# Performance work log

Measured on AMD Instinct MI355X. Metric: run time of the kernel, lower is better.

The kernel has to match this reference:

```python
import jax, jax.numpy as jnp
import numpy as np

NC = 3
NA = 3
NO2D = NC + 5
BIN = 2
NO3D = BIN * 3 + 3
STRIDES = (8.0, 16.0, 32.0)
ANCHORS = np.array([[10, 13, 16, 30, 33, 23],
                    [30, 61, 62, 45, 59, 119],
                    [116, 90, 156, 198, 373, 326]], np.float32).reshape(3, NA, 2)
IN_CHES = (256, 512, 1024)
SIZES = ((80, 80), (40, 40), (20, 20))
BS = 8


def _conv(x, w, b, pad):
    y = jax.lax.conv_general_dilated(x, w, (1, 1), ((pad, pad), (pad, pad)),
                                     dimension_numbers=('NCHW', 'OIHW', 'NCHW'))
    return y + b[None, :, None, None]


def setup_inputs() -> dict:
    key = jax.random.key(0)
    d = {}
    k = [0]
    def nk():
        k[0] += 1
        return jax.random.fold_in(key, k[0])
    for i, (c, (ny, nx)) in enumerate(zip(IN_CHES, SIZES)):
        d[f"f{i}"] = jax.random.normal(nk(), (BS, c, ny, nx), jnp.float32)
        d[f"w2a{i}"] = jax.random.normal(nk(), (c, c, 3, 3), jnp.float32) * 0.01
        d[f"b2a{i}"] = jnp.zeros((c,), jnp.float32)
        d[f"w2b{i}"] = jax.random.normal(nk(), (NA * NO2D, c, 1, 1), jnp.float32) * 0.01
        d[f"b2b{i}"] = jnp.zeros((NA * NO2D,), jnp.float32)
        d[f"w3a{i}"] = jax.random.normal(nk(), (c, c, 3, 3), jnp.float32) * 0.01
        d[f"b3a{i}"] = jnp.zeros((c,), jnp.float32)
        d[f"w3b{i}"] = jax.random.normal(nk(), (NA * NO3D, c, 1, 1), jnp.float32) * 0.01
        d[f"b3b{i}"] = jnp.zeros((NA * NO3D,), jnp.float32)
    return d


def _decode(feats, params):
    anchors = jnp.asarray(ANCHORS)  # [L, NA, 2]
    preds = []
    for i in range(3):
        x = feats[i]
        w2a, b2a, w2b, b2b, w3a, b3a, w3b, b3b = params[i]
        # detection heads: 3x3 conv -> 1x1 conv
        h2 = _conv(_conv(x, w2a, b2a, 1), w2b, b2b, 0)  # [bs, na*NO2D, ny, nx]
        h3 = _conv(_conv(x, w3a, b3a, 1), w3b, b3b, 0)  # [bs, na*NO3D, ny, nx]
        bs, _, ny, nx = h2.shape
        h2 = h2.reshape(bs, NA, NO2D, ny, nx).transpose(0, 1, 3, 4, 2)  # [bs,na,ny,nx,NO2D]
        h3 = h3.reshape(bs, NA, NO3D, ny, nx).transpose(0, 1, 3, 4, 2).reshape(bs, -1, NO3D)
        # 2d decode
        p2 = jax.nn.sigmoid(h2)
        yv, xv = jnp.meshgrid(jnp.arange(ny, dtype=jnp.float32),
                              jnp.arange(nx, dtype=jnp.float32), indexing='ij')
        grid = jnp.stack((xv, yv), -1)[None, None]  # [1,1,ny,nx,2]
        xy = (p2[..., 0:2] * 2.0 - 0.5 + grid) * STRIDES[i]
        wh = (p2[..., 2:4] * 2.0) ** 2 * anchors[i][None, :, None, None, :]
        p2 = jnp.concatenate([xy, wh, p2[..., 4:]], -1).reshape(bs, -1, NO2D)
        # 3d decode: bin confidences raw, bin orients L2-normalized, dims sigmoid*2-1
        bins = h3[..., :BIN]
        orient = h3[..., BIN:3 * BIN].reshape(bs, -1, BIN, 2)
        norm = jnp.maximum(jnp.linalg.norm(orient, axis=-1, keepdims=True), 1e-12)
        orient = (orient / norm).reshape(bs, -1, BIN * 2)
        dims = jax.nn.sigmoid(h3[..., -3:]) * 2.0 - 1.0
        p3 = jnp.concatenate([bins, orient, dims], -1)
        preds.append(jnp.concatenate([p2, p3], -1))
    return jnp.concatenate(preds, 1)  # [bs, 25200, NO2D+NO3D]


def reference(f0, f1, f2,
              w2a0, b2a0, w2b0, b2b0, w3a0, b3a0, w3b0, b3b0,
              w2a1, b2a1, w2b1, b2b1, w3a1, b3a1, w3b1, b3b1,
              w2a2, b2a2, w2b2, b2b2, w3a2, b3a2, w3b2, b3b2):
    feats = (f0, f1, f2)
    params = ((w2a0, b2a0, w2b0, b2b0, w3a0, b3a0, w3b0, b3b0),
              (w2a1, b2a1, w2b1, b2b1, w3a1, b3a1, w3b1, b3b1),
              (w2a2, b2a2, w2b2, b2b2, w3a2, b3a2, w3b2, b3b2))
    return _decode(feats, params)
```

## Files before the change

### kernel.cpp

```cpp
#include <hip/hip_runtime.h>
#include <hip/hip_bf16.h>
#include <cstddef>
#include <cstdint>
#include <climits>

#define TOT_ANCH 25200

typedef __bf16 bf16x8 __attribute__((ext_vector_type(8)));
typedef float f32x4 __attribute__((ext_vector_type(4)));

__device__ __forceinline__ float sig_(float x) { return 1.0f / (1.0f + __expf(-x)); }

__device__ __forceinline__ short f2bf(float v) {
  return (short)__builtin_bit_cast(unsigned short, __float2bfloat16(v));
}
__device__ __forceinline__ float bf2f(short v) {
  unsigned int u = ((unsigned int)(unsigned short)v) << 16;
  return __builtin_bit_cast(float, u);
}
__device__ __forceinline__ bf16x8 as_bf16x8(int4 v) { return __builtin_bit_cast(bf16x8, v); }

__device__ __forceinline__ void gload_lds16(const void* g, void* l) {
  __builtin_amdgcn_global_load_lds((const __attribute__((address_space(1))) void*)g,
                                   (__attribute__((address_space(3))) void*)l, 16, 0, 0);
}

__device__ const float d_anch[3][3][2] = {
    {{10.f, 13.f}, {16.f, 30.f}, {33.f, 23.f}},
    {{30.f, 61.f}, {62.f, 45.f}, {59.f, 119.f}},
    {{116.f, 90.f}, {156.f, 198.f}, {373.f, 326.f}}};

struct TrP {
  const float* f; short* fb; int C, HW, ptiles, c32, blk0;
};
struct WtP {
  const float* w; short* dst; long CC, MC, off0; int blk0;
};
struct WcP {
  const float* w2b; const float* w3b; short* wc; int csh2, blk0;
};
struct ConvP {
  const short* fb; const short* wt; const float* bA; const float* bB; short* h;
  int C, H, W, HW, nb_m, nwg, mfast, blk0;
};
struct DeP {
  const short* h; const short* wc; const float* bb2; const float* bb3;
  int C2, H, W, b0, loff, ptiles, lvl, blk0; float stride;
};

__global__ __launch_bounds__(256) void aux_mega(TrP T0, TrP T1, TrP T2,
                                                WtP J0, WtP J1, WtP J2,
                                                WtP J3, WtP J4, WtP J5, int wt_blk0) {
  __shared__ short tile[32][33];
  int bid = blockIdx.x;
  if (bid >= wt_blk0) {
    WtP J = bid >= J5.blk0 ? J5 : bid >= J4.blk0 ? J4 : bid >= J3.blk0 ? J3 :
            bid >= J2.blk0 ? J2 : bid >= J1.blk0 ? J1 : J0;
    long oi = (long)(bid - J.blk0) * 256 + threadIdx.x;
    if (oi >= J.CC) return;
#pragma unroll
    for (int t = 0; t < 9; ++t) J.dst[t * J.MC + J.off0 + oi] = f2bf(J.w[oi * 9 + t]);
    return;
  }
  TrP T = bid >= T2.blk0 ? T2 : (bid >= T1.blk0 ? T1 : T0);
  int l = bid - T.blk0;
  const int pt = l % T.ptiles; l /= T.ptiles;
  const int cg = l % T.c32;
  const int b = l / T.c32;
  const int p0 = pt * 32, c0 = cg * 32, HW = T.HW, C = T.C;
  const int t = threadIdx.x;
  {
    int cl = t >> 3, pl = (t & 7) * 4;
    int pr = p0 + pl;
    if (pr > HW - 4) pr = HW - 4;
    const float4 v = *(const float4*)(T.f + ((long)b * C + c0 + cl) * HW + pr);
    tile[cl][pl + 0] = f2bf(v.x);
    tile[cl][pl + 1] = f2bf(v.y);
    tile[cl][pl + 2] = f2bf(v.z);
    tile[cl][pl + 3] = f2bf(v.w);
  }
  __syncthreads();
  {
    int pl = t >> 3, cl = (t & 7) * 4;
    int pp = p0 + pl;
    if (pp < HW) {
      int k = pl >> 2;
      int start = p0 + 4 * k;
      if (start > HW - 4) start = HW - 4;
      int col = (start - p0) + (pp - start);
      short4 o;
      o.x = tile[cl + 0][col];
      o.y = tile[cl + 1][col];
      o.z = tile[cl + 2][col];
      o.w = tile[cl + 3][col];
      *(short4*)(T.fb + ((long)b * HW + pp) * C + c0 + cl) = o;
    }
  }
}

__global__ __launch_bounds__(256) void wc_prep(WcP K0, WcP K1, WcP K2) {
  int bid = blockIdx.x;
  WcP K = bid >= K2.blk0 ? K2 : (bid >= K1.blk0 ? K1 : K0);
  int idx = (bid - K.blk0) * 256 + threadIdx.x;
  const int C2 = 1 << K.csh2;
  if (idx >= 64 * C2) return;
  const int row = idx >> K.csh2;
  const int c = idx & (C2 - 1);
  const int C = C2 >> 1;
  float v = 0.f;
  if (row < 24) {
    if (c < C) v = K.w2b[row * C + c];
  } else if (row < 51) {
    if (c >= C) v = K.w3b[(row - 24) * C + (c - C)];
  }
  K.wc[idx] = f2bf(v);
}

__global__ __launch_bounds__(256, 3) void conv3x3_mega(ConvP P0, ConvP P1, ConvP P2,
                                                       const short* zbuf) {
  __shared__ __align__(16) short As[128 * 64];
  __shared__ __align__(16) short Xs[128 * 64];

  int bid = blockIdx.x;
  ConvP P = bid >= P2.blk0 ? P2 : (bid >= P1.blk0 ? P1 : P0);
  const int C = P.C, H = P.H, W = P.W, HW = P.HW, nb_m = P.nb_m, nwg = P.nwg;

  const int orig = bid - P.blk0;
  const int q = nwg >> 3, rr = nwg & 7;
  const int xcd = orig & 7;
  const int wg = (xcd < rr ? xcd * (q + 1) : rr * (q + 1) + (xcd - rr) * q) + (orig >> 3);
  int m, n;
  if (P.mfast) { m = wg % nb_m; n = wg / nb_m; }
  else         { const int nb_n = nwg / nb_m; n = wg % nb_n; m = wg / nb_n; }
  const int mt0 = m * 128;
  const int nt0 = n * 128;
  const int M2 = nb_m * 128;

  const int tid = threadIdx.x;
  const int lane = tid & 63;
  const int wave = tid >> 6;
  const int wm = (wave >> 1) * 64;
  const int wn = (wave & 1) * 64;
  const int s = tid & 7;

  int xs_x[4], xs_y[4];
  int xs_base[4];
  int as_base[4];
#pragma unroll
  for (int r = 0; r < 4; ++r) {
    int cl = r * 32 + (tid >> 3);
    int nn = nt0 + cl;
    int b = nn / HW; int p = nn - b * HW;
    int y = p / W;  int x = p - y * W;
    xs_x[r] = x; xs_y[r] = y;
    int swz = (s ^ (cl & 7)) * 8;
    xs_base[r] = ((b * H + y) * W + x) * C + swz;
    as_base[r] = (mt0 + cl) * C + swz;
  }

  f32x4 acc[4][4];
#pragma unroll
  for (int a_ = 0; a_ < 4; ++a_)
#pragma unroll
    for (int b_ = 0; b_ < 4; ++b_) acc[a_][b_] = (f32x4){0.f, 0.f, 0.f, 0.f};

  const int nkb = C >> 6;
  const long MC = (long)M2 * C;
  const short* gzb = zbuf + s * 8;

  for (int kb = 0; kb < nkb; ++kb) {
    const int kb64 = kb << 6;
    for (int t = 0; t < 9; ++t) {
      const int dy = t / 3 - 1, dx = t - (t / 3) * 3 - 1;
      const int doff = (dy * W + dx) * C + kb64;
      const short* gap = P.wt + (long)t * MC + kb64;
#pragma unroll
      for (int r = 0; r < 4; ++r) {
        gload_lds16(gap + as_base[r], (char*)As + r * 4096 + tid * 16);
        bool ok = ((unsigned)(xs_y[r] + dy) < (unsigned)H) &
                  ((unsigned)(xs_x[r] + dx) < (unsigned)W);
        const short* gx = ok ? P.fb + xs_base[r] + doff : gzb;
        gload_lds16(gx, (char*)Xs + r * 4096 + tid * 16);
      }
      __syncthreads();

#pragma unroll
      for (int ks = 0; ks < 2; ++ks) {
        bf16x8 af[4], xf[4];
#pragma unroll
        for (int mf = 0; mf < 4; ++mf) {
          int row = wm + mf * 16 + (lane & 15);
          int c = (ks * 4 + (lane >> 4)) ^ (row & 7);
          af[mf] = as_bf16x8(*(const int4*)((const char*)As + row * 128 + c * 16));
        }
#pragma unroll
        for (int nf = 0; nf < 4; ++nf) {
          int col = wn + nf * 16 + (lane & 15);
          int c = (ks * 4 + (lane >> 4)) ^ (col & 7);
          xf[nf] = as_bf16x8(*(const int4*)((const char*)Xs + col * 128 + c * 16));
        }
        __builtin_amdgcn_s_setprio(1);
#pragma unroll
        for (int mf = 0; mf < 4; ++mf)
#pragma unroll
          for (int nf = 0; nf < 4; ++nf)
            acc[mf][nf] = __builtin_amdgcn_mfma_f32_16x16x32_bf16(af[mf], xf[nf],
                                                                  acc[mf][nf], 0, 0, 0);
        __builtin_amdgcn_s_setprio(0);
      }
      __syncthreads();
    }
  }

  long nbase[4];
#pragma unroll
  for (int nf = 0; nf < 4; ++nf) {
    int nn = nt0 + wn + nf * 16 + (lane & 15);
    int nb = nn / HW;
    int np = nn - nb * HW;
    nbase[nf] = ((long)nb * HW + np) * M2;
  }
#pragma unroll
  for (int mf = 0; mf < 4; ++mf) {
    int co0 = mt0 + wm + mf * 16 + (lane >> 4) * 4;
    float bv[4];
#pragma unroll
    for (int rg = 0; rg < 4; ++rg) {
      int co = co0 + rg;
      bv[rg] = co < C ? P.bA[co] : P.bB[co - C];
    }
#pragma unroll
    for (int nf = 0; nf < 4; ++nf) {
      short4 o;
      o.x = f2bf(acc[mf][nf][0] + bv[0]);
      o.y = f2bf(acc[mf][nf][1] + bv[1]);
      o.z = f2bf(acc[mf][nf][2] + bv[2]);
      o.w = f2bf(acc[mf][nf][3] + bv[3]);
      *(short4*)(P.h + nbase[nf] + co0) = o;
    }
  }
}

__global__ __launch_bounds__(256) void decode_v3(DeP D0, DeP D1, DeP D2,
                                                 float* __restrict__ out) {
  __shared__ __align__(16) short htileT[32][136];
  __shared__ __align__(16) short Wtile[64][136];
  __shared__ float otile[32][52];
  int bid = blockIdx.x;
  DeP D = bid >= D2.blk0 ? D2 : (bid >= D1.blk0 ? D1 : D0);
  int l = bid - D.blk0;
  const int pt = l % D.ptiles;
  const int bl = l / D.ptiles;
  const int C2 = D.C2, H = D.H, W = D.W, HW = H * W;
  const int t = threadIdx.x;
  const int lane = t & 63;
  const int wv = t >> 6;
  const int p0 = pt * 32;

  const short* hB = D.h + (long)bl * HW * C2;

  f32x4 acc[2];
  acc[0] = (f32x4){0.f, 0.f, 0.f, 0.f};
  acc[1] = (f32x4){0.f, 0.f, 0.f, 0.f};

  const int rounds = C2 >> 7;
  for (int rd = 0; rd < rounds; ++rd) {
    const int c0 = rd << 7;
#pragma unroll
    for (int r = 0; r < 2; ++r) {
      int idx = r * 256 + t;
      int px = idx >> 4, kc = idx & 15;
      int p = p0 + px;
      int pc = p < HW ? p : HW - 1;
      int4 v = *(const int4*)(hB + (long)pc * C2 + c0 + kc * 8);
      *(int4*)&htileT[px][kc * 8] = v;
    }
#pragma unroll
    for (int r = 0; r < 4; ++r) {
      int idx = r * 256 + t;
      int row = idx >> 4, kc = idx & 15;
      int4 v = *(const int4*)(D.wc + (long)row * C2 + c0 + kc * 8);
      *(int4*)&Wtile[row][kc * 8] = v;
    }
    __syncthreads();
#pragma unroll
    for (int st = 0; st < 4; ++st) {
      const int k0 = st * 32 + (lane >> 4) * 8;
      bf16x8 af = as_bf16x8(*(const int4*)&Wtile[wv * 16 + (lane & 15)][k0]);
#pragma unroll
      for (int nf = 0; nf < 2; ++nf) {
        bf16x8 xf = as_bf16x8(*(const int4*)&htileT[nf * 16 + (lane & 15)][k0]);
        acc[nf] = __builtin_amdgcn_mfma_f32_16x16x32_bf16(af, xf, acc[nf], 0, 0, 0);
      }
    }
    __syncthreads();
  }

#pragma unroll
  for (int nf = 0; nf < 2; ++nf) {
    int px = nf * 16 + (lane & 15);
#pragma unroll
    for (int rg = 0; rg < 4; ++rg) {
      int row = wv * 16 + (lane >> 4) * 4 + rg;
      if (row < 51) otile[px][row] = acc[nf][rg];
    }
  }
  __syncthreads();

  if (t < 96) {
    const int pxx = t / 3, a = t - (t / 3) * 3;
    const int p = p0 + pxx;
    if (p < HW) {
      float* o = out + ((size_t)(D.b0 + bl) * TOT_ANCH + D.loff + (size_t)a * HW + p) * 17;
      {
        const int y = p / W, x = p - (p / W) * W;
        float h0 = otile[pxx][a * 8 + 0] + D.bb2[a * 8 + 0];
        float h1 = otile[pxx][a * 8 + 1] + D.bb2[a * 8 + 1];
        float h2 = otile[pxx][a * 8 + 2] + D.bb2[a * 8 + 2];
        float h3 = otile[pxx][a * 8 + 3] + D.bb2[a * 8 + 3];
        float s0 = sig_(h0);
        float s1 = sig_(h1);
        float sw = sig_(h2) * 2.f;
        float sh = sig_(h3) * 2.f;
        o[0] = (s0 * 2.f - 0.5f + (float)x) * D.stride;
        o[1] = (s1 * 2.f - 0.5f + (float)y) * D.stride;
        o[2] = sw * sw * d_anch[D.lvl][a][0];
        o[3] = sh * sh * d_anch[D.lvl][a][1];
        o[4] = sig_(otile[pxx][a * 8 + 4] + D.bb2[a * 8 + 4]);
        o[5] = sig_(otile[pxx][a * 8 + 5] + D.bb2[a * 8 + 5]);
        o[6] = sig_(otile[pxx][a * 8 + 6] + D.bb2[a * 8 + 6]);
        o[7] = sig_(otile[pxx][a * 8 + 7] + D.bb2[a * 8 + 7]);
      }
      {
        float v0 = otile[pxx][24 + a * 9 + 0] + D.bb3[a * 9 + 0];
        float v1 = otile[pxx][24 + a * 9 + 1] + D.bb3[a * 9 + 1];
        float v2 = otile[pxx][24 + a * 9 + 2] + D.bb3[a * 9 + 2];
        float v3 = otile[pxx][24 + a * 9 + 3] + D.bb3[a * 9 + 3];
        float v4 = otile[pxx][24 + a * 9 + 4] + D.bb3[a * 9 + 4];
        float v5 = otile[pxx][24 + a * 9 + 5] + D.bb3[a * 9 + 5];
        float v6 = otile[pxx][24 + a * 9 + 6] + D.bb3[a * 9 + 6];
        float v7 = otile[pxx][24 + a * 9 + 7] + D.bb3[a * 9 + 7];
        float v8 = otile[pxx][24 + a * 9 + 8] + D.bb3[a * 9 + 8];
        float n0 = fmaxf(sqrtf(v2 * v2 + v3 * v3), 1e-12f);
        float n1 = fmaxf(sqrtf(v4 * v4 + v5 * v5), 1e-12f);
        o[8] = v0;
        o[9] = v1;
        o[10] = v2 / n0;
        o[11] = v3 / n0;
        o[12] = v4 / n1;
        o[13] = v5 / n1;
        o[14] = sig_(v6) * 2.f - 1.f;
        o[15] = sig_(v7) * 2.f - 1.f;
        o[16] = sig_(v8) * 2.f - 1.f;
      }
    }
  }
}


static inline size_t al256(size_t x) { return (x + 255) & ~(size_t)255; }

extern "C" void kernel_launch(void* const* d_in, const int* in_sizes, int n_in,
                              void* d_out, int out_size, void* d_ws, size_t ws_size,
                              hipStream_t stream) {
  (void)in_sizes; (void)n_in; (void)out_size;
  char* ws = (char*)d_ws;
  float* out = (float*)d_out;

  hipMemsetAsync(ws, 0, 256, stream);
  const short* zb = (const short*)ws;

  struct Lvl { int C, H, W, loff; float stride; };
  const Lvl L[3] = {{256, 80, 80, 0, 8.f}, {512, 40, 40, 19200, 16.f},
                    {1024, 20, 20, 24000, 32.f}};
  const int B = 8;
  const int ord[3] = {2, 1, 0};

  const float* f_[3]; const float *w2a_[3], *b2a_[3], *w2b_[3], *b2b_[3];
  const float *w3a_[3], *b3a_[3], *w3b_[3], *b3b_[3];
  int HW_[3], ptiles_[3], c32_[3], nbm_[3], mfast_[3], csh2_[3];
  long CC_[3];
  size_t fbB_[3], wtB_[3], hB_[3], wcB_[3];
  for (int i = 0; i < 3; ++i) {
    f_[i]   = (const float*)d_in[9 * i + 0];
    w2a_[i] = (const float*)d_in[9 * i + 1];
    b2a_[i] = (const float*)d_in[9 * i + 2];
    w2b_[i] = (const float*)d_in[9 * i + 3];
    b2b_[i] = (const float*)d_in[9 * i + 4];
    w3a_[i] = (const float*)d_in[9 * i + 5];
    b3a_[i] = (const float*)d_in[9 * i + 6];
    w3b_[i] = (const float*)d_in[9 * i + 7];
    b3b_[i] = (const float*)d_in[9 * i + 8];
    const int C = L[i].C;
    HW_[i] = L[i].H * L[i].W;
    ptiles_[i] = (HW_[i] + 31) / 32;
    c32_[i] = C / 32;
    nbm_[i] = (2 * C) / 128;
    CC_[i] = (long)C * C;
    csh2_[i] = (C == 256) ? 9 : (C == 512) ? 10 : 11;
    fbB_[i] = (size_t)B * HW_[i] * C * 2;
    wtB_[i] = (size_t)36 * CC_[i];
    hB_[i]  = (size_t)B * HW_[i] * 2 * C * 2;
    wcB_[i] = (size_t)64 * 2 * C * 2;
    mfast_[i] = ((size_t)B * HW_[i] * C >= (size_t)18 * CC_[i]) ? 1 : 0;
  }

  size_t off = 256;
  size_t fb_o[3], wt_o[3], h_o[3], wc_o[3];
  for (int i = 0; i < 3; ++i) { fb_o[i] = off; off += al256(fbB_[i]); }
  for (int i = 0; i < 3; ++i) { wt_o[i] = off; off += al256(wtB_[i]); }
  for (int i = 0; i < 3; ++i) { wc_o[i] = off; off += al256(wcB_[i]); }
  for (int i = 0; i < 3; ++i) { h_o[i] = off; off += al256(hB_[i]); }

  if (off <= ws_size) {
    short* fb[3]; short* wtb[3]; short* hb[3]; short* wcb[3];
    for (int i = 0; i < 3; ++i) {
      fb[i] = (short*)(ws + fb_o[i]);
      wtb[i] = (short*)(ws + wt_o[i]);
      hb[i] = (short*)(ws + h_o[i]);
      wcb[i] = (short*)(ws + wc_o[i]);
    }
    TrP T[3]; int tb = 0;
    for (int i = 0; i < 3; ++i) {
      T[i] = TrP{f_[i], fb[i], L[i].C, HW_[i], ptiles_[i], c32_[i], tb};
      tb += ptiles_[i] * c32_[i] * B;
    }
    WtP J[6]; int jb = tb;
    for (int i = 0; i < 3; ++i) {
      J[2 * i]     = WtP{w2a_[i], wtb[i], CC_[i], 2 * CC_[i], 0, jb};
      jb += (int)(CC_[i] / 256);
      J[2 * i + 1] = WtP{w3a_[i], wtb[i], CC_[i], 2 * CC_[i], CC_[i], jb};
      jb += (int)(CC_[i] / 256);
    }
    aux_mega<<<jb, 256, 0, stream>>>(T[0], T[1], T[2], J[0], J[1], J[2], J[3], J[4],
                                     J[5], tb);
    WcP K[3]; int kb = 0;
    for (int i = 0; i < 3; ++i) {
      K[i] = WcP{w2b_[i], w3b_[i], wcb[i], csh2_[i], kb};
      kb += (64 * 2 * L[i].C) / 256;
    }
    wc_prep<<<kb, 256, 0, stream>>>(K[0], K[1], K[2]);

    ConvP P[3]; int cb = 0;
    for (int k = 0; k < 3; ++k) {
      const int i = ord[k];
      int nwg = (B * HW_[i] / 128) * nbm_[i];
      P[k] = ConvP{fb[i], wtb[i], b2a_[i], b3a_[i], hb[i],
                   L[i].C, L[i].H, L[i].W, HW_[i], nbm_[i], nwg, mfast_[i], cb};
      cb += nwg;
    }
    conv3x3_mega<<<cb, 256, 0, stream>>>(P[0], P[1], P[2], zb);

    DeP D[3]; int db = 0;
    for (int k = 0; k < 3; ++k) {
      const int i = ord[k];
      D[k] = DeP{hb[i], wcb[i], b2b_[i], b3b_[i], 2 * L[i].C, L[i].H, L[i].W,
                 0, L[i].loff, ptiles_[i], i, db, L[i].stride};
      db += ptiles_[i] * B;
    }
    decode_v3<<<db, 256, 0, stream>>>(D[0], D[1], D[2], out);
    return;
  }

  for (int i = 0; i < 3; ++i) {
    const int C = L[i].C, HW = HW_[i];
    int Bg = B;
    for (int cand = 1; cand <= 8; cand <<= 1) {
      int bg = B / cand;
      if (((long)bg * HW) % 128) continue;
      size_t need = 256 + al256((size_t)bg * HW * C * 2) + al256(wtB_[i]) +
                    al256(wcB_[i]) + (size_t)bg * HW * 2 * C * 2;
      if (need <= ws_size) { Bg = bg; break; }
    }
    size_t fo = 256;
    size_t wo = fo + al256((size_t)Bg * HW * C * 2);
    size_t co = wo + al256(wtB_[i]);
    size_t ho = co + al256(wcB_[i]);
    short* fb = (short*)(ws + fo);
    short* wtb = (short*)(ws + wo);
    short* wcb = (short*)(ws + co);
    short* hb = (short*)(ws + ho);

    TrP TZ{};
    WtP J0 = WtP{w2a_[i], wtb, CC_[i], 2 * CC_[i], 0, 0};
    WtP J1 = WtP{w3a_[i], wtb, CC_[i], 2 * CC_[i], CC_[i], (int)(CC_[i] / 256)};
    WtP JX = J1; JX.blk0 = INT_MAX;
    aux_mega<<<(int)(2 * CC_[i] / 256), 256, 0, stream>>>(TZ, TZ, TZ, J0, J1, JX, JX,
                                                          JX, JX, 0);
    WcP K0 = WcP{w2b_[i], w3b_[i], wcb, csh2_[i], 0};
    WcP KX = K0; KX.blk0 = INT_MAX;
    wc_prep<<<(64 * 2 * C) / 256, 256, 0, stream>>>(K0, KX, KX);

    const int nbg = B / Bg;
    for (int g = 0; g < nbg; ++g) {
      const int b0 = g * Bg;
      TrP T0 = TrP{f_[i] + (size_t)b0 * C * HW, fb, C, HW, ptiles_[i], c32_[i], 0};
      TrP TX = T0; TX.blk0 = INT_MAX;
      WtP JZ{}; JZ.blk0 = INT_MAX;
      aux_mega<<<ptiles_[i] * c32_[i] * Bg, 256, 0, stream>>>(T0, TX, TX, JZ, JZ, JZ,
                                                              JZ, JZ, JZ, INT_MAX);

      int nwg = (Bg * HW / 128) * nbm_[i];
      ConvP Pc = ConvP{fb, wtb, b2a_[i], b3a_[i], hb, C, L[i].H, L[i].W, HW,
                       nbm_[i], nwg, mfast_[i], 0};
      ConvP PX = Pc; PX.blk0 = INT_MAX;
      conv3x3_mega<<<nwg, 256, 0, stream>>>(Pc, PX, PX, zb);

      DeP D0 = DeP{hb, wcb, b2b_[i], b3b_[i], 2 * C, L[i].H, L[i].W,
                   b0, L[i].loff, ptiles_[i], i, 0, L[i].stride};
      DeP DX = D0; DX.blk0 = INT_MAX;
      decode_v3<<<ptiles_[i] * Bg, 256, 0, stream>>>(D0, DX, DX, out);
    }
  }
}
```

Measured before the change: 423.0 us.

## Enlarge conv tiles to 256x256 with double-buffered LDS prefetch pipeline

Reworks the implicit-GEMM 3x3 conv to use 512-thread blocks computing 256x256 output tiles. LDS is double-buffered in 32-wide K halves, and the next tap's global-to-LDS loads are issued in phases between MFMA groups, with explicit waitcnt and barriers. N tiles are now bounds-checked so sizes no longer need to divide the tile, and the XCD remapping is simplified. The aim is more data reuse per tile and less load latency exposed at barriers. The cost is higher register pressure (32 accumulators per lane), more LDS per block, and fewer blocks for the small levels, which may leave CUs underfilled.

Result: slower. 469.2 us (+10.9%).

```diff
diff --git a/kernel.cpp b/kernel.cpp
--- a/kernel.cpp
+++ b/kernel.cpp
@@ -41,7 +41,7 @@
 };
 struct ConvP {
   const short* fb; const short* wt; const float* bA; const float* bB; short* h;
-  int C, H, W, HW, nb_m, nwg, mfast, blk0;
+  int C, H, W, HW, Ng, nb_m, nwg, mfast, blk0;
 };
 struct DeP {
   const short* h; const short* wc; const float* bb2; const float* bb3;
@@ -116,113 +116,154 @@
   K.wc[idx] = f2bf(v);
 }
 
-__global__ __launch_bounds__(256, 3) void conv3x3_mega(ConvP P0, ConvP P1, ConvP P2,
-                                                       const short* zbuf) {
-  __shared__ __align__(16) short As[128 * 64];
-  __shared__ __align__(16) short Xs[128 * 64];
+__global__ __launch_bounds__(512) void conv3x3_mega(ConvP P0, ConvP P1, ConvP P2,
+                                                    const short* zbuf) {
+  __shared__ __align__(16) short As[2][2][256 * 32];
+  __shared__ __align__(16) short Xs[2][2][256 * 32];
 
   int bid = blockIdx.x;
   ConvP P = bid >= P2.blk0 ? P2 : (bid >= P1.blk0 ? P1 : P0);
-  const int C = P.C, H = P.H, W = P.W, HW = P.HW, nb_m = P.nb_m, nwg = P.nwg;
+  const int C = P.C, H = P.H, W = P.W, HW = P.HW, Ng = P.Ng;
+  const int nb_m = P.nb_m, nwg = P.nwg;
 
   const int orig = bid - P.blk0;
-  const int q = nwg >> 3, rr = nwg & 7;
-  const int xcd = orig & 7;
-  const int wg = (xcd < rr ? xcd * (q + 1) : rr * (q + 1) + (xcd - rr) * q) + (orig >> 3);
+  int wg;
+  if (nwg & 7) wg = orig;
+  else { const int q = nwg >> 3; wg = (orig & 7) * q + (orig >> 3); }
   int m, n;
   if (P.mfast) { m = wg % nb_m; n = wg / nb_m; }
   else         { const int nb_n = nwg / nb_m; n = wg % nb_n; m = wg / nb_n; }
-  const int mt0 = m * 128;
-  const int nt0 = n * 128;
-  const int M2 = nb_m * 128;
+  const int mt0 = m * 256;
+  const int nt0 = n * 256;
+  const int M2 = nb_m * 256;
 
   const int tid = threadIdx.x;
   const int lane = tid & 63;
   const int wave = tid >> 6;
-  const int wm = (wave >> 1) * 64;
-  const int wn = (wave & 1) * 64;
-  const int s = tid & 7;
-
-  int xs_x[4], xs_y[4];
-  int xs_base[4];
-  int as_base[4];
-#pragma unroll
-  for (int r = 0; r < 4; ++r) {
-    int cl = r * 32 + (tid >> 3);
-    int nn = nt0 + cl;
-    int b = nn / HW; int p = nn - b * HW;
-    int y = p / W;  int x = p - y * W;
-    xs_x[r] = x; xs_y[r] = y;
-    int swz = (s ^ (cl & 7)) * 8;
-    xs_base[r] = ((b * H + y) * W + x) * C + swz;
-    as_base[r] = (mt0 + cl) * C + swz;
-  }
-
-  f32x4 acc[4][4];
-#pragma unroll
-  for (int a_ = 0; a_ < 4; ++a_)
+  const int wm = wave >> 2;
+  const int wn = wave & 3;
+
+  const int srow0 = tid >> 2;
+  const int swzc = ((tid & 3) ^ ((tid >> 3) & 3)) * 8;
+  int xs_x[2], xs_y[2], xs_vld[2];
+  long xs_base[2], as_base[2];
+#pragma unroll
+  for (int r = 0; r < 2; ++r) {
+    int row = r * 128 + srow0;
+    int nn = nt0 + row;
+    int vld = nn < Ng;
+    int nnc = vld ? nn : 0;
+    int b = nnc / HW; int p = nnc - b * HW;
+    int y = p / W;    int x = p - y * W;
+    xs_x[r] = x; xs_y[r] = y; xs_vld[r] = vld;
+    xs_base[r] = (long)((b * H + y) * W + x) * C + swzc;
+    as_base[r] = (long)(mt0 + row) * C + swzc;
+  }
+
+  f32x4 acc[8][4];
+#pragma unroll
+  for (int a_ = 0; a_ < 8; ++a_)
 #pragma unroll
     for (int b_ = 0; b_ < 4; ++b_) acc[a_][b_] = (f32x4){0.f, 0.f, 0.f, 0.f};
 
   const int nkb = C >> 6;
+  const int nkt = nkb * 9;
   const long MC = (long)M2 * C;
-  const short* gzb = zbuf + s * 8;
-
-  for (int kb = 0; kb < nkb; ++kb) {
-    const int kb64 = kb << 6;
-    for (int t = 0; t < 9; ++t) {
-      const int dy = t / 3 - 1, dx = t - (t / 3) * 3 - 1;
-      const int doff = (dy * W + dx) * C + kb64;
-      const short* gap = P.wt + (long)t * MC + kb64;
-#pragma unroll
-      for (int r = 0; r < 4; ++r) {
-        gload_lds16(gap + as_base[r], (char*)As + r * 4096 + tid * 16);
-        bool ok = ((unsigned)(xs_y[r] + dy) < (unsigned)H) &
-                  ((unsigned)(xs_x[r] + dx) < (unsigned)W);
-        const short* gx = ok ? P.fb + xs_base[r] + doff : gzb;
-        gload_lds16(gx, (char*)Xs + r * 4096 + tid * 16);
-      }
-      __syncthreads();
-
-#pragma unroll
-      for (int ks = 0; ks < 2; ++ks) {
-        bf16x8 af[4], xf[4];
-#pragma unroll
-        for (int mf = 0; mf < 4; ++mf) {
-          int row = wm + mf * 16 + (lane & 15);
-          int c = (ks * 4 + (lane >> 4)) ^ (row & 7);
-          af[mf] = as_bf16x8(*(const int4*)((const char*)As + row * 128 + c * 16));
+  const short* gzb = zbuf + swzc;
+
+  auto SA = [&](int db, int kh, const short* wtap, int kb64) {
+#pragma unroll
+    for (int r = 0; r < 2; ++r)
+      gload_lds16(wtap + as_base[r] + kb64 + kh * 32,
+                  (char*)&As[db][kh][0] + r * 8192 + tid * 16);
+  };
+  auto SX = [&](int db, int kh, int dy, int dx, int doff) {
+#pragma unroll
+    for (int r = 0; r < 2; ++r) {
+      bool ok = xs_vld[r] && ((unsigned)(xs_y[r] + dy) < (unsigned)H) &&
+                ((unsigned)(xs_x[r] + dx) < (unsigned)W);
+      const short* gx = ok ? P.fb + xs_base[r] + doff + kh * 32 : gzb;
+      gload_lds16(gx, (char*)&Xs[db][kh][0] + r * 8192 + tid * 16);
+    }
+  };
+
+  {
+    const int doff0 = (-W - 1) * C;
+    SA(0, 0, P.wt, 0);
+    SX(0, 0, -1, -1, doff0);
+    SA(0, 1, P.wt, 0);
+    SX(0, 1, -1, -1, doff0);
+  }
+
+  int ntt = 1, nkb64 = 0;
+  for (int kt = 0; kt < nkt; ++kt) {
+    const int cur = kt & 1;
+    const int nxt = cur ^ 1;
+    const bool hasn = (kt + 1) < nkt;
+    const int td3 = ntt / 3;
+    const int dyn = td3 - 1, dxn = ntt - td3 * 3 - 1;
+    const int doffn = (dyn * W + dxn) * C + nkb64;
+    const short* wtapn = P.wt + (long)ntt * MC;
+
+    bf16x8 xf[4];
+#pragma unroll
+    for (int ph = 0; ph < 4; ++ph) {
+      const int ks = ph >> 1, mh = ph & 1;
+      if (mh == 0) {
+        asm volatile("s_waitcnt vmcnt(4)" ::: "memory");
+        __builtin_amdgcn_sched_barrier(0);
+        __builtin_amdgcn_s_barrier();
+      }
+      if (hasn) {
+        if (ph == 0)      SA(nxt, 0, wtapn, nkb64);
+        else if (ph == 1) SX(nxt, 0, dyn, dxn, doffn);
+        else if (ph == 2) SA(nxt, 1, wtapn, nkb64);
+        else              SX(nxt, 1, dyn, dxn, doffn);
+      }
+      const char* Ah = (const char*)&As[cur][ks][0];
+      const char* Xh = (const char*)&Xs[cur][ks][0];
+      if (mh == 0) {
+#pragma unroll
+        for (int nf = 0; nf < 4; ++nf) {
+          int rl = wn * 64 + nf * 16 + (lane & 15);
+          int c = (lane >> 4) ^ ((rl >> 1) & 3);
+          xf[nf] = as_bf16x8(*(const int4*)(Xh + rl * 64 + c * 16));
         }
-#pragma unroll
-        for (int nf = 0; nf < 4; ++nf) {
-          int col = wn + nf * 16 + (lane & 15);
-          int c = (ks * 4 + (lane >> 4)) ^ (col & 7);
-          xf[nf] = as_bf16x8(*(const int4*)((const char*)Xs + col * 128 + c * 16));
-        }
-        __builtin_amdgcn_s_setprio(1);
-#pragma unroll
-        for (int mf = 0; mf < 4; ++mf)
-#pragma unroll
-          for (int nf = 0; nf < 4; ++nf)
-            acc[mf][nf] = __builtin_amdgcn_mfma_f32_16x16x32_bf16(af[mf], xf[nf],
-                                                                  acc[mf][nf], 0, 0, 0);
-        __builtin_amdgcn_s_setprio(0);
-      }
-      __syncthreads();
-    }
-  }
-
-  long nbase[4];
+      }
+      bf16x8 af[4];
+#pragma unroll
+      for (int mf = 0; mf < 4; ++mf) {
+        int rl = wm * 128 + mh * 64 + mf * 16 + (lane & 15);
+        int c = (lane >> 4) ^ ((rl >> 1) & 3);
+        af[mf] = as_bf16x8(*(const int4*)(Ah + rl * 64 + c * 16));
+      }
+      asm volatile("s_waitcnt lgkmcnt(0)" ::: "memory");
+      __builtin_amdgcn_sched_barrier(0);
+      __builtin_amdgcn_s_setprio(1);
+#pragma unroll
+      for (int mf = 0; mf < 4; ++mf)
+#pragma unroll
+        for (int nf = 0; nf < 4; ++nf)
+          acc[mh * 4 + mf][nf] = __builtin_amdgcn_mfma_f32_16x16x32_bf16(
+              af[mf], xf[nf], acc[mh * 4 + mf][nf], 0, 0, 0);
+      __builtin_amdgcn_s_setprio(0);
+    }
+    if (++ntt == 9) { ntt = 0; nkb64 += 64; }
+  }
+
+  long nbase[4]; int nok[4];
 #pragma unroll
   for (int nf = 0; nf < 4; ++nf) {
-    int nn = nt0 + wn + nf * 16 + (lane & 15);
-    int nb = nn / HW;
-    int np = nn - nb * HW;
+    int nn = nt0 + wn * 64 + nf * 16 + (lane & 15);
+    nok[nf] = nn < Ng;
+    int nnc = nok[nf] ? nn : 0;
+    int nb = nnc / HW;
+    int np = nnc - nb * HW;
     nbase[nf] = ((long)nb * HW + np) * M2;
   }
 #pragma unroll
-  for (int mf = 0; mf < 4; ++mf) {
-    int co0 = mt0 + wm + mf * 16 + (lane >> 4) * 4;
+  for (int g = 0; g < 8; ++g) {
+    int co0 = mt0 + wm * 128 + (g >> 2) * 64 + (g & 3) * 16 + (lane >> 4) * 4;
     float bv[4];
 #pragma unroll
     for (int rg = 0; rg < 4; ++rg) {
@@ -231,12 +272,14 @@
     }
 #pragma unroll
     for (int nf = 0; nf < 4; ++nf) {
-      short4 o;
-      o.x = f2bf(acc[mf][nf][0] + bv[0]);
-      o.y = f2bf(acc[mf][nf][1] + bv[1]);
-      o.z = f2bf(acc[mf][nf][2] + bv[2]);
-      o.w = f2bf(acc[mf][nf][3] + bv[3]);
-      *(short4*)(P.h + nbase[nf] + co0) = o;
+      if (nok[nf]) {
+        short4 o;
+        o.x = f2bf(acc[g][nf][0] + bv[0]);
+        o.y = f2bf(acc[g][nf][1] + bv[1]);
+        o.z = f2bf(acc[g][nf][2] + bv[2]);
+        o.w = f2bf(acc[g][nf][3] + bv[3]);
+        *(short4*)(P.h + nbase[nf] + co0) = o;
+      }
     }
   }
 }
@@ -395,7 +438,7 @@
     HW_[i] = L[i].H * L[i].W;
     ptiles_[i] = (HW_[i] + 31) / 32;
     c32_[i] = C / 32;
-    nbm_[i] = (2 * C) / 128;
+    nbm_[i] = (2 * C) / 256;
     CC_[i] = (long)C * C;
     csh2_[i] = (C == 256) ? 9 : (C == 512) ? 10 : 11;
     fbB_[i] = (size_t)B * HW_[i] * C * 2;
@@ -444,12 +487,14 @@
     ConvP P[3]; int cb = 0;
     for (int k = 0; k < 3; ++k) {
       const int i = ord[k];
-      int nwg = (B * HW_[i] / 128) * nbm_[i];
+      const int Ng = B * HW_[i];
+      const int ntn = (Ng + 255) / 256;
+      const int nwg = ntn * nbm_[i];
       P[k] = ConvP{fb[i], wtb[i], b2a_[i], b3a_[i], hb[i],
-                   L[i].C, L[i].H, L[i].W, HW_[i], nbm_[i], nwg, mfast_[i], cb};
+                   L[i].C, L[i].H, L[i].W, HW_[i], Ng, nbm_[i], nwg, mfast_[i], cb};
       cb += nwg;
     }
-    conv3x3_mega<<<cb, 256, 0, stream>>>(P[0], P[1], P[2], zb);
+    conv3x3_mega<<<cb, 512, 0, stream>>>(P[0], P[1], P[2], zb);
 
     DeP D[3]; int db = 0;
     for (int k = 0; k < 3; ++k) {
@@ -467,7 +512,6 @@
     int Bg = B;
     for (int cand = 1; cand <= 8; cand <<= 1) {
       int bg = B / cand;
-      if (((long)bg * HW) % 128) continue;
       size_t need = 256 + al256((size_t)bg * HW * C * 2) + al256(wtB_[i]) +
                     al256(wcB_[i]) + (size_t)bg * HW * 2 * C * 2;
       if (need <= ws_size) { Bg = bg; break; }
@@ -500,11 +544,13 @@
       aux_mega<<<ptiles_[i] * c32_[i] * Bg, 256, 0, stream>>>(T0, TX, TX, JZ, JZ, JZ,
                                                               JZ, JZ, JZ, INT_MAX);
 
-      int nwg = (Bg * HW / 128) * nbm_[i];
+      const int Ng = Bg * HW;
+      const int ntn = (Ng + 255) / 256;
+      const int nwg = ntn * nbm_[i];
       ConvP Pc = ConvP{fb, wtb, b2a_[i], b3a_[i], hb, C, L[i].H, L[i].W, HW,
-                       nbm_[i], nwg, mfast_[i], 0};
+                       Ng, nbm_[i], nwg, mfast_[i], 0};
       ConvP PX = Pc; PX.blk0 = INT_MAX;
-      conv3x3_mega<<<nwg, 256, 0, stream>>>(Pc, PX, PX, zb);
+      conv3x3_mega<<<nwg, 512, 0, stream>>>(Pc, PX, PX, zb);
 
       DeP D0 = DeP{hb, wcb, b2b_[i], b3b_[i], 2 * C, L[i].H, L[i].W,
                    b0, L[i].loff, ptiles_[i], i, 0, L[i].stride};
```
